# Kernel optimization log

Hardware: AMD Instinct MI355X
Metric: run time of the kernel (lower is better)

## Reference

```python
import jax, jax.numpy as jnp
import numpy as np

DIM = 1024
NUM_HEADS = 16
HEAD_DIM = DIM // NUM_HEADS


def setup_inputs() -> dict:
    key = jax.random.key(0)
    k1, k2, k3 = jax.random.split(key, 3)
    scale = 1.0 / np.sqrt(DIM)
    x = jax.random.normal(k1, (4, 2048, DIM), dtype=jnp.float32)
    w_qkv = jax.random.normal(k2, (DIM, 3 * DIM), dtype=jnp.float32) * scale
    b_qkv = jnp.zeros((3 * DIM,), dtype=jnp.float32)
    w_out = jax.random.normal(k3, (DIM, DIM), dtype=jnp.float32) * scale
    b_out = jnp.zeros((DIM,), dtype=jnp.float32)
    return {"x": x, "w_qkv": w_qkv, "b_qkv": b_qkv, "w_out": w_out, "b_out": b_out}


def reference(x, w_qkv, b_qkv, w_out, b_out):
    B, S, D = x.shape
    H, Hd = NUM_HEADS, HEAD_DIM
    qkv = x @ w_qkv + b_qkv  # [B,S,3D]
    q, k, v = jnp.split(qkv, 3, axis=-1)
    # [B,H,S,Hd]
    q = q.reshape(B, S, H, Hd).transpose(0, 2, 1, 3)
    k = k.reshape(B, S, H, Hd).transpose(0, 2, 1, 3)
    v = v.reshape(B, S, H, Hd).transpose(0, 2, 1, 3)
    scores = jnp.einsum('bhqd,bhkd->bhqk', q, k) / np.sqrt(Hd).astype(np.float32)
    causal = jnp.triu(jnp.ones((S, S), dtype=bool), k=1)  # True above diagonal -> masked
    scores = jnp.where(causal[None, None], -jnp.inf, scores)
    scores = scores - jnp.max(scores, axis=-1, keepdims=True)
    attn = jax.nn.softmax(scores, axis=-1)
    out = jnp.einsum('bhqk,bhkd->bhqd', attn, v)  # [B,H,S,Hd]
    out = out.transpose(0, 2, 1, 3).reshape(B, S, D)
    return out @ w_out + b_out
```

## Files before the change

### kernel.cpp

```cpp
#include <hip/hip_runtime.h>

typedef unsigned short u16;
typedef unsigned int u32;
using f32x4 = __attribute__((ext_vector_type(4))) float;
using f32x16 = __attribute__((ext_vector_type(16))) float;
using u32x4 = __attribute__((ext_vector_type(4))) u32;
typedef u32x4 __attribute__((may_alias)) u32x4a;
typedef uint2 __attribute__((may_alias)) uint2a;
using bf16x8 = __attribute__((ext_vector_type(8))) __bf16;

#define SEQ 2048

__device__ __forceinline__ u16 f2bf(float f) {
  union { float f; u32 u; } c; c.f = f;
  return (u16)((c.u + 0x7fffu + ((c.u >> 16) & 1u)) >> 16);
}
__device__ __forceinline__ float bf2f(u16 h) {
  union { u32 u; float f; } c; c.u = ((u32)h) << 16;
  return c.f;
}
__device__ __forceinline__ bf16x8 ld16(const u16* p) {
  return __builtin_bit_cast(bf16x8, *(const u32x4a*)p);
}
__device__ __forceinline__ f32x4 mfma16(bf16x8 a, bf16x8 b, f32x4 c) {
  return __builtin_amdgcn_mfma_f32_16x16x32_bf16(a, b, c, 0, 0, 0);
}
__device__ __forceinline__ f32x16 mfma32(bf16x8 a, bf16x8 b, f32x16 c) {
  return __builtin_amdgcn_mfma_f32_32x32x16_bf16(a, b, c, 0, 0, 0);
}
__device__ __forceinline__ void gload_lds16(const u16* g, u16* l) {
  __builtin_amdgcn_global_load_lds(
      (const __attribute__((address_space(1))) void*)g,
      (__attribute__((address_space(3))) void*)l, 16, 0, 0);
}
__device__ __forceinline__ u32 cvtpk(float lo, float hi) {
  u32 r;
  asm("v_cvt_pk_bf16_f32 %0, %1, %2" : "=v"(r) : "v"(lo), "v"(hi));
  return r;
}
__device__ __forceinline__ void plane32_swap(u32& a, u32& b) {
  asm("v_permlane32_swap_b32 %0, %1" : "+v"(a), "+v"(b));
}

__global__ void detect_dtype(const u16* __restrict__ x, int* __restrict__ flag) {
  if (threadIdx.x == 0) {
    int cnt = 0;
    for (int i = 0; i < 32; ++i) {
      const int e = (x[2 * i] >> 7) & 0xFF;
      cnt += (e >= 100 && e <= 140) ? 1 : 0;
    }
    *flag = (cnt >= 20) ? 1 : 0;
  }
}


__global__ __launch_bounds__(256)
void cvt_x(const void* __restrict__ in, u16* __restrict__ out,
           const int* __restrict__ flag, size_t eoff4) {
  const size_t i = (size_t)blockIdx.x * 256 + threadIdx.x;
  if (*flag) {
    ((uint2*)out)[i] = ((const uint2*)in)[eoff4 + i];
  } else {
    const float4 v = ((const float4*)in)[eoff4 + i];
    uint2 ov;
    ov.x = (u32)f2bf(v.x) | ((u32)f2bf(v.y) << 16);
    ov.y = (u32)f2bf(v.z) | ((u32)f2bf(v.w) << 16);
    ((uint2*)out)[i] = ov;
  }
}

__global__ __launch_bounds__(256)
void cvt_bias(const void* __restrict__ in, float* __restrict__ out, int n,
              const int* __restrict__ flag) {
  const int i = blockIdx.x * 256 + threadIdx.x;
  if (i >= n) return;
  out[i] = (*flag) ? bf2f(((const u16*)in)[i]) : ((const float*)in)[i];
}

__global__ __launch_bounds__(256)
void transpose_w(const void* __restrict__ in, u16* __restrict__ out, int K, int N,
                 const int* __restrict__ flag) {
  __shared__ float t[64][65];
  const int tid = threadIdx.x;
  const int r = tid >> 4, c4 = tid & 15;
  const int n0 = blockIdx.x << 6, k0 = blockIdx.y << 6;
  const int fl = *flag;
#pragma unroll
  for (int i = 0; i < 4; ++i) {
    const int kk = r + i * 16;
    const size_t base = (size_t)(k0 + kk) * N + n0 + c4 * 4;
    if (fl) {
      const uint2 raw = *(const uint2*)((const u16*)in + base);
      t[kk][c4 * 4 + 0] = bf2f((u16)(raw.x & 0xFFFF));
      t[kk][c4 * 4 + 1] = bf2f((u16)(raw.x >> 16));
      t[kk][c4 * 4 + 2] = bf2f((u16)(raw.y & 0xFFFF));
      t[kk][c4 * 4 + 3] = bf2f((u16)(raw.y >> 16));
    } else {
      const float4 v = *(const float4*)((const float*)in + base);
      t[kk][c4 * 4 + 0] = v.x; t[kk][c4 * 4 + 1] = v.y;
      t[kk][c4 * 4 + 2] = v.z; t[kk][c4 * 4 + 3] = v.w;
    }
  }
  __syncthreads();
#pragma unroll
  for (int i = 0; i < 4; ++i) {
    const int nn = r + i * 16;
    uint2 ov;
    ov.x = (u32)f2bf(t[c4 * 4 + 0][nn]) | ((u32)f2bf(t[c4 * 4 + 1][nn]) << 16);
    ov.y = (u32)f2bf(t[c4 * 4 + 2][nn]) | ((u32)f2bf(t[c4 * 4 + 3][nn]) << 16);
    *(uint2*)&out[(size_t)(n0 + nn) * K + k0 + c4 * 4] = ov;
  }
}

template <bool BF16_OUT>
__global__ __launch_bounds__(512, 4)
void gemm_bt(const u16* __restrict__ A, const u16* __restrict__ BT,
             const float* __restrict__ bias, void* __restrict__ Cv,
             u16* __restrict__ Vt, int M, int N, int K) {
  constexpr int BK = 32;
  __shared__ __align__(16) u16 ring[3][12288];
  const int tid = threadIdx.x;
  const int wid = tid >> 6, lane = tid & 63;
  const int quad = lane >> 4, l16 = lane & 15;

  const int nbx = gridDim.x, nwg = nbx * gridDim.y;
  int bid = blockIdx.y * nbx + blockIdx.x;
  if ((nwg & 7) == 0) bid = (bid & 7) * (nwg >> 3) + (bid >> 3);
  const int tile_n = (bid % nbx) << 7;
  const int tile_m = (bid / nbx) << 8;

  const int wmR = (wid >> 1) << 6;
  const int wnR = (wid & 1) << 6;

  const int G0 = tid;
  const int rA0 = G0 >> 2, sA0 = ((G0 & 3) ^ ((rA0 >> 1) & 3)) * 8;
  const int G1 = tid + 512;
  const int rA1 = G1 >> 2, sA1 = ((G1 & 3) ^ ((rA1 >> 1) & 3)) * 8;
  const u16* const pA0 = A + (size_t)(tile_m + rA0) * K + sA0;
  const u16* const pA1 = A + (size_t)(tile_m + rA1) * K + sA1;
  const u16* const pB0 = BT + (size_t)(tile_n + rA0) * K + sA0;
  const int dw = wid * 512;

  const int cA = (quad ^ ((l16 >> 1) & 3)) * 8;

  const int nk = K >> 5;
  f32x4 acc[4][4] = {};

  auto STAGE = [&](int kt, int buf) {
    u16* bp = ring[buf];
    const size_t ko = (size_t)kt * BK;
    gload_lds16(pA0 + ko, bp + dw);
    gload_lds16(pA1 + ko, bp + 4096 + dw);
    gload_lds16(pB0 + ko, bp + 8192 + dw);
  };

  STAGE(0, 0);
  if (nk > 1) STAGE(1, 1);

  int cur = 0;
#pragma unroll 1
  for (int t = 0; t < nk; ++t) {
    if (t + 1 < nk) asm volatile("s_waitcnt vmcnt(3)" ::: "memory");
    else            asm volatile("s_waitcnt vmcnt(0)" ::: "memory");
    __builtin_amdgcn_sched_barrier(0);
    __builtin_amdgcn_s_barrier();
    __builtin_amdgcn_sched_barrier(0);
    int sb = cur + 2; if (sb >= 3) sb -= 3;
    if (t + 2 < nk) STAGE(t + 2, sb);
    const u16* bp = ring[cur];
    bf16x8 af[4], bfr[4];
#pragma unroll
    for (int i = 0; i < 4; ++i)
      af[i] = ld16(&bp[(wmR + i * 16 + l16) * BK + cA]);
#pragma unroll
    for (int j = 0; j < 4; ++j)
      bfr[j] = ld16(&bp[8192 + (wnR + j * 16 + l16) * BK + cA]);
#pragma unroll
    for (int i = 0; i < 4; ++i)
#pragma unroll
      for (int j = 0; j < 4; ++j) acc[i][j] = mfma16(af[i], bfr[j], acc[i][j]);
    cur = (cur + 1 == 3) ? 0 : cur + 1;
  }

  if constexpr (BF16_OUT) {
    if (tile_n >= 2048) {
#pragma unroll
      for (int j = 0; j < 4; ++j) {
        const int cv = tile_n - 2048 + wnR + j * 16 + l16;
        const float bv = bias[2048 + cv];
#pragma unroll
        for (int i = 0; i < 4; ++i) {
          const int rg = tile_m + wmR + i * 16 + quad * 4;
          const int b2 = rg >> 11, s = rg & 2047;
          uint2a wv;
          wv.x = cvtpk(acc[i][j][0] + bv, acc[i][j][1] + bv);
          wv.y = cvtpk(acc[i][j][2] + bv, acc[i][j][3] + bv);
          *(uint2a*)&Vt[((size_t)(b2 * 1024 + cv)) * 2048 + s] = wv;
        }
      }
      return;
    }
  }

#pragma unroll
  for (int j = 0; j < 4; ++j) {
    const int cg = tile_n + wnR + j * 16 + l16;
    const float bv = bias[cg];
#pragma unroll
    for (int i = 0; i < 4; ++i) {
      const int rg = tile_m + wmR + i * 16 + quad * 4;
#pragma unroll
      for (int r = 0; r < 4; ++r) {
        const float v = acc[i][j][r] + bv;
        if constexpr (BF16_OUT)
          ((u16*)Cv)[(size_t)(rg + r) * N + cg] = f2bf(v);
        else
          ((float*)Cv)[(size_t)(rg + r) * N + cg] = v;
      }
    }
  }
}

__global__ __launch_bounds__(256, 2)
void attn_fwd(const u16* __restrict__ qkv, const u16* __restrict__ vt,
              u16* __restrict__ aout) {
  const int h = blockIdx.x, b = blockIdx.z;
  const int tid = threadIdx.x, wid = tid >> 6, lane = tid & 63;
  const int l31 = lane & 31, hi = lane >> 5;
  __shared__ __align__(16) u16 ring[4][8192];

  const int G0 = wid * 64 + lane, G1 = G0 + 256;
  const int r0 = G0 >> 3, c0 = ((G0 & 7) ^ (r0 & 7)) * 8;
  const int r1 = G1 >> 3, c1 = ((G1 & 7) ^ (r1 & 7)) * 8;
  const int db0 = wid * 512, db1 = 2048 + wid * 512;

  const u16* const kg = qkv + (size_t)(b * SEQ) * 3072 + 1024 + h * 64;
  const u16* const vg = vt + (size_t)((b * 16 + h) * 64) * 2048;

  constexpr float SC = 0.1803368801f;
  constexpr float THR = 44.3614196f;

  u32x4 onesu;
  onesu[0] = onesu[1] = onesu[2] = onesu[3] = 0x3F803F80u;
  const bf16x8 ones = __builtin_bit_cast(bf16x8, onesu);

  const int sx = l31 & 7;

  auto STAGE = [&](int kt) {
    u16* bp = ring[kt & 3];
    const int kb = kt * 64;
    gload_lds16(kg + (size_t)(kb + r0) * 3072 + c0, bp + db0);
    gload_lds16(kg + (size_t)(kb + r1) * 3072 + c1, bp + db1);
    gload_lds16(vg + (size_t)r0 * 2048 + kb + c0, bp + 4096 + db0);
    gload_lds16(vg + (size_t)r1 * 2048 + kb + c1, bp + 4096 + db1);
  };

#pragma unroll 1
  for (int pass = 0; pass < 2; ++pass) {
    const int qt = pass ? (int)blockIdx.y : 15 - (int)blockIdx.y;
    const int q0w = qt * 128 + wid * 32;
    const int qrow = q0w + l31;
    bf16x8 qf[4];
#pragma unroll
    for (int d = 0; d < 4; ++d)
      qf[d] = ld16(&qkv[(size_t)(b * SEQ + qrow) * 3072 + h * 64 + d * 16 + hi * 8]);
    f32x16 o0 = {}, o1 = {}, lacc = {};
    float m_r = -1e30f, ms = -1.8e29f;

    const int last = 2 * qt + 1;
    __syncthreads();
    STAGE(0);
    if (last >= 1) STAGE(1);
    if (last >= 2) STAGE(2);

#pragma unroll 1
    for (int kt = 0; kt <= last; ++kt) {
      const int rem = last - kt;
      if (rem >= 2)      asm volatile("s_waitcnt vmcnt(8)" ::: "memory");
      else if (rem == 1) asm volatile("s_waitcnt vmcnt(4)" ::: "memory");
      else               asm volatile("s_waitcnt vmcnt(0)" ::: "memory");
      __builtin_amdgcn_sched_barrier(0);
      __builtin_amdgcn_s_barrier();
      __builtin_amdgcn_sched_barrier(0);
      if (kt + 3 <= last) STAGE(kt + 3);
      const int kb = kt * 64;
      if (kb <= q0w + 31) {
        const u16* const lKc = ring[kt & 3];
        const u16* const lVc = ring[kt & 3] + 4096;
        f32x16 s0 = {}, s1 = {};
        bf16x8 kf0[4], kf1[4];
#pragma unroll
        for (int d = 0; d < 4; ++d) {
          kf0[d] = ld16(&lKc[l31 * 64 + (((d * 2 + hi) ^ sx)) * 8]);
          kf1[d] = ld16(&lKc[(32 + l31) * 64 + (((d * 2 + hi) ^ sx)) * 8]);
        }
        __builtin_amdgcn_s_setprio(1);
#pragma unroll
        for (int d = 0; d < 4; ++d) s0 = mfma32(kf0[d], qf[d], s0);
#pragma unroll
        for (int d = 0; d < 4; ++d) s1 = mfma32(kf1[d], qf[d], s1);
        __builtin_amdgcn_s_setprio(0);
        bf16x8 vf[2][2][2];
#pragma unroll
        for (int kh = 0; kh < 2; ++kh)
#pragma unroll
          for (int j = 0; j < 2; ++j)
#pragma unroll
            for (int dh = 0; dh < 2; ++dh)
              vf[kh][j][dh] = ld16(
                  &lVc[(dh * 32 + l31) * 64 + (((kh * 4 + j * 2 + hi) ^ sx)) * 8]);
        if (kb + 63 > q0w) {
          const int rel = qrow - kb - 4 * hi;
#pragma unroll
          for (int i = 0; i < 16; ++i) {
            const int kc = (i & 3) + 8 * (i >> 2);
            if (kc > rel) s0[i] = -1e30f;
            if (kc + 32 > rel) s1[i] = -1e30f;
          }
        }
        float pm = fmaxf(fmaxf(s0[0], s0[1]), s0[2]);
        pm = fmaxf(fmaxf(pm, s0[3]), s0[4]);
        pm = fmaxf(fmaxf(pm, s0[5]), s0[6]);
        pm = fmaxf(fmaxf(pm, s0[7]), s0[8]);
        pm = fmaxf(fmaxf(pm, s0[9]), s0[10]);
        pm = fmaxf(fmaxf(pm, s0[11]), s0[12]);
        pm = fmaxf(fmaxf(pm, s0[13]), s0[14]);
        pm = fmaxf(fmaxf(pm, s0[15]), s1[0]);
        pm = fmaxf(fmaxf(pm, s1[1]), s1[2]);
        pm = fmaxf(fmaxf(pm, s1[3]), s1[4]);
        pm = fmaxf(fmaxf(pm, s1[5]), s1[6]);
        pm = fmaxf(fmaxf(pm, s1[7]), s1[8]);
        pm = fmaxf(fmaxf(pm, s1[9]), s1[10]);
        pm = fmaxf(fmaxf(pm, s1[11]), s1[12]);
        pm = fmaxf(fmaxf(pm, s1[13]), s1[14]);
        pm = fmaxf(pm, s1[15]);
        if (__any(pm > m_r + THR)) {
          const float mm = fmaxf(pm, __shfl_xor(pm, 32));
          const float mn = fmaxf(m_r, mm);
          const float al = exp2f((m_r - mn) * SC);
#pragma unroll
          for (int i = 0; i < 16; ++i) {
            o0[i] *= al; o1[i] *= al; lacc[i] *= al;
          }
          m_r = mn;
          ms = mn * SC;
        }
#pragma unroll
        for (int i = 0; i < 16; ++i) {
          s0[i] = exp2f(fmaf(s0[i], SC, -ms));
          s1[i] = exp2f(fmaf(s1[i], SC, -ms));
        }
        u32 t0 = cvtpk(s0[0], s0[1]), t1 = cvtpk(s0[2], s0[3]);
        u32 t2 = cvtpk(s0[4], s0[5]), t3 = cvtpk(s0[6], s0[7]);
        u32 t4 = cvtpk(s0[8], s0[9]), t5 = cvtpk(s0[10], s0[11]);
        u32 t6 = cvtpk(s0[12], s0[13]), t7 = cvtpk(s0[14], s0[15]);
        plane32_swap(t0, t2); plane32_swap(t1, t3);
        plane32_swap(t4, t6); plane32_swap(t5, t7);
        u32x4 w00, w01;
        w00[0] = t0; w00[1] = t1; w00[2] = t2; w00[3] = t3;
        w01[0] = t4; w01[1] = t5; w01[2] = t6; w01[3] = t7;
        u32 u0 = cvtpk(s1[0], s1[1]), u1 = cvtpk(s1[2], s1[3]);
        u32 u2 = cvtpk(s1[4], s1[5]), u3 = cvtpk(s1[6], s1[7]);
        u32 u4 = cvtpk(s1[8], s1[9]), u5 = cvtpk(s1[10], s1[11]);
        u32 u6 = cvtpk(s1[12], s1[13]), u7 = cvtpk(s1[14], s1[15]);
        plane32_swap(u0, u2); plane32_swap(u1, u3);
        plane32_swap(u4, u6); plane32_swap(u5, u7);
        u32x4 w10, w11;
        w10[0] = u0; w10[1] = u1; w10[2] = u2; w10[3] = u3;
        w11[0] = u4; w11[1] = u5; w11[2] = u6; w11[3] = u7;
        const bf16x8 pb00 = __builtin_bit_cast(bf16x8, w00);
        const bf16x8 pb01 = __builtin_bit_cast(bf16x8, w01);
        const bf16x8 pb10 = __builtin_bit_cast(bf16x8, w10);
        const bf16x8 pb11 = __builtin_bit_cast(bf16x8, w11);
        __builtin_amdgcn_s_setprio(1);
        o0 = mfma32(vf[0][0][0], pb00, o0);
        o1 = mfma32(vf[0][0][1], pb00, o1);
        lacc = mfma32(ones, pb00, lacc);
        o0 = mfma32(vf[0][1][0], pb01, o0);
        o1 = mfma32(vf[0][1][1], pb01, o1);
        lacc = mfma32(ones, pb01, lacc);
        o0 = mfma32(vf[1][0][0], pb10, o0);
        o1 = mfma32(vf[1][0][1], pb10, o1);
        lacc = mfma32(ones, pb10, lacc);
        o0 = mfma32(vf[1][1][0], pb11, o0);
        o1 = mfma32(vf[1][1][1], pb11, o1);
        lacc = mfma32(ones, pb11, lacc);
        __builtin_amdgcn_s_setprio(0);
      }
    }
    const float inv = 1.0f / lacc[0];
    u16* const orow = &aout[(size_t)(b * SEQ + qrow) * 1024 + h * 64];
#pragma unroll
    for (int t = 0; t < 4; ++t) {
      const int d0 = 8 * t + 4 * hi;
      uint2a wv;
      wv.x = cvtpk(o0[4 * t] * inv, o0[4 * t + 1] * inv);
      wv.y = cvtpk(o0[4 * t + 2] * inv, o0[4 * t + 3] * inv);
      *(uint2a*)&orow[d0] = wv;
      wv.x = cvtpk(o1[4 * t] * inv, o1[4 * t + 1] * inv);
      wv.y = cvtpk(o1[4 * t + 2] * inv, o1[4 * t + 3] * inv);
      *(uint2a*)&orow[32 + d0] = wv;
    }
  }
}

extern "C" void kernel_launch(void* const* d_in, const int* in_sizes, int n_in,
                              void* d_out, int out_size, void* d_ws, size_t ws_size,
                              hipStream_t stream) {
  const void* x     = d_in[0];
  const void* w_qkv = d_in[1];
  const void* b_qkv = d_in[2];
  const void* w_out = d_in[3];
  const void* b_out = d_in[4];
  float* out = (float*)d_out;

  float* bqf   = (float*)d_ws;
  float* bof   = bqf + 3072;
  int*   flag  = (int*)(bof + 1024);
  u16*   wqkvT = (u16*)(flag + 4);
  u16*   woutT = wqkvT + (size_t)3072 * 1024;
  u16*   xb    = woutT + (size_t)1024 * 1024;

  detect_dtype<<<dim3(1), dim3(64), 0, stream>>>((const u16*)x, flag);
  cvt_bias<<<dim3(12), dim3(256), 0, stream>>>(b_qkv, bqf, 3072, flag);
  cvt_bias<<<dim3(4), dim3(256), 0, stream>>>(b_out, bof, 1024, flag);
  transpose_w<<<dim3(48, 16), dim3(256), 0, stream>>>(w_qkv, wqkvT, 1024, 3072, flag);
  transpose_w<<<dim3(16, 16), dim3(256), 0, stream>>>(w_out, woutT, 1024, 1024, flag);

  const size_t FULL_WS = 92291088;
  if (ws_size >= FULL_WS) {
    u16* qkv = xb  + (size_t)8192 * 1024;
    u16* vt  = qkv + (size_t)8192 * 3072;
    cvt_x<<<dim3(8192), dim3(256), 0, stream>>>(x, xb, flag, 0);
    gemm_bt<true ><<<dim3(24, 32), dim3(512), 0, stream>>>(xb, wqkvT, bqf, qkv,
                                                           vt, 8192, 3072, 1024);
    attn_fwd<<<dim3(16, 8, 4), dim3(256), 0, stream>>>(qkv, vt, xb);
    gemm_bt<false><<<dim3(8, 32), dim3(512), 0, stream>>>(xb, woutT, bof, out,
                                                          vt, 8192, 1024, 1024);
  } else {
    u16* qkvb = xb   + (size_t)2048 * 1024;
    u16* vtb  = qkvb + (size_t)2048 * 3072;
    for (int b = 0; b < 4; ++b) {
      const size_t eoff4 = (size_t)b * 2048 * 1024 / 4;
      cvt_x<<<dim3(2048), dim3(256), 0, stream>>>(x, xb, flag, eoff4);
      gemm_bt<true ><<<dim3(24, 8), dim3(512), 0, stream>>>(xb, wqkvT, bqf, qkvb,
                                                            vtb, 2048, 3072, 1024);
      attn_fwd<<<dim3(16, 8, 1), dim3(256), 0, stream>>>(qkvb, vtb, xb);
      gemm_bt<false><<<dim3(8, 8), dim3(512), 0, stream>>>(
          xb, woutT, bof, out + (size_t)b * 2048 * 1024, vtb, 2048, 1024, 1024);
    }
  }
}
```

Baseline: 277.5 us.

## Split attention blocks per query tile, shrink LDS ring, fuse prep kernels

Attention no longer pairs two query tiles per block (long+short for balance). It launches one block per query tile (grid y 16) with the tiles ordered longest first. The LDS ring drops from 4 to 3 stages with prefetch distance 2, allowing 3 blocks per CU. The five small preprocessing kernels (dtype detection, bias conversion, weight transposes) are merged into one launch, and each block recomputes the dtype flag locally. The risks are lost load balance from the pairing and a shallower prefetch pipeline.

```diff
diff --git a/kernel.cpp b/kernel.cpp
--- a/kernel.cpp
+++ b/kernel.cpp
@@ -41,50 +41,50 @@
 __device__ __forceinline__ void plane32_swap(u32& a, u32& b) {
   asm("v_permlane32_swap_b32 %0, %1" : "+v"(a), "+v"(b));
 }
-
-__global__ void detect_dtype(const u16* __restrict__ x, int* __restrict__ flag) {
-  if (threadIdx.x == 0) {
-    int cnt = 0;
-    for (int i = 0; i < 32; ++i) {
-      const int e = (x[2 * i] >> 7) & 0xFF;
-      cnt += (e >= 100 && e <= 140) ? 1 : 0;
-    }
-    *flag = (cnt >= 20) ? 1 : 0;
-  }
-}
-
+__device__ __forceinline__ int detect_flag(const u16* x) {
+  int cnt = 0;
+  for (int i = 0; i < 32; ++i) {
+    const int e = (x[2 * i] >> 7) & 0xFF;
+    cnt += (e >= 100 && e <= 140) ? 1 : 0;
+  }
+  return (cnt >= 20) ? 1 : 0;
+}
 
 __global__ __launch_bounds__(256)
-void cvt_x(const void* __restrict__ in, u16* __restrict__ out,
-           const int* __restrict__ flag, size_t eoff4) {
-  const size_t i = (size_t)blockIdx.x * 256 + threadIdx.x;
-  if (*flag) {
-    ((uint2*)out)[i] = ((const uint2*)in)[eoff4 + i];
-  } else {
-    const float4 v = ((const float4*)in)[eoff4 + i];
-    uint2 ov;
-    ov.x = (u32)f2bf(v.x) | ((u32)f2bf(v.y) << 16);
-    ov.y = (u32)f2bf(v.z) | ((u32)f2bf(v.w) << 16);
-    ((uint2*)out)[i] = ov;
-  }
-}
-
-__global__ __launch_bounds__(256)
-void cvt_bias(const void* __restrict__ in, float* __restrict__ out, int n,
-              const int* __restrict__ flag) {
-  const int i = blockIdx.x * 256 + threadIdx.x;
-  if (i >= n) return;
-  out[i] = (*flag) ? bf2f(((const u16*)in)[i]) : ((const float*)in)[i];
-}
-
-__global__ __launch_bounds__(256)
-void transpose_w(const void* __restrict__ in, u16* __restrict__ out, int K, int N,
-                 const int* __restrict__ flag) {
+void prep_all(const void* __restrict__ x, const void* __restrict__ w_qkv,
+              const void* __restrict__ b_qkv, const void* __restrict__ w_out,
+              const void* __restrict__ b_out, u16* __restrict__ wqkvT,
+              u16* __restrict__ woutT, float* __restrict__ bqf,
+              float* __restrict__ bof, int* __restrict__ flagp) {
+  __shared__ int sflag;
   __shared__ float t[64][65];
   const int tid = threadIdx.x;
+  if (tid == 0) sflag = detect_flag((const u16*)x);
+  __syncthreads();
+  const int fl = sflag;
+  const int bid = blockIdx.x;
+  if (bid == 1040) {
+    if (tid == 0) *flagp = fl;
+    return;
+  }
+  if (bid >= 1024) {
+    if (bid < 1036) {
+      const int i = (bid - 1024) * 256 + tid;
+      bqf[i] = fl ? bf2f(((const u16*)b_qkv)[i]) : ((const float*)b_qkv)[i];
+    } else {
+      const int i = (bid - 1036) * 256 + tid;
+      bof[i] = fl ? bf2f(((const u16*)b_out)[i]) : ((const float*)b_out)[i];
+    }
+    return;
+  }
+  const void* in;
+  u16* outp;
+  int N, bx, by;
+  if (bid < 768) { in = w_qkv; outp = wqkvT; N = 3072; bx = bid % 48; by = bid / 48; }
+  else { in = w_out; outp = woutT; N = 1024; bx = (bid - 768) % 16; by = (bid - 768) / 16; }
+  const int K = 1024;
   const int r = tid >> 4, c4 = tid & 15;
-  const int n0 = blockIdx.x << 6, k0 = blockIdx.y << 6;
-  const int fl = *flag;
+  const int n0 = bx << 6, k0 = by << 6;
 #pragma unroll
   for (int i = 0; i < 4; ++i) {
     const int kk = r + i * 16;
@@ -108,7 +108,22 @@
     uint2 ov;
     ov.x = (u32)f2bf(t[c4 * 4 + 0][nn]) | ((u32)f2bf(t[c4 * 4 + 1][nn]) << 16);
     ov.y = (u32)f2bf(t[c4 * 4 + 2][nn]) | ((u32)f2bf(t[c4 * 4 + 3][nn]) << 16);
-    *(uint2*)&out[(size_t)(n0 + nn) * K + k0 + c4 * 4] = ov;
+    *(uint2*)&outp[(size_t)(n0 + nn) * K + k0 + c4 * 4] = ov;
+  }
+}
+
+__global__ __launch_bounds__(256)
+void cvt_x(const void* __restrict__ in, u16* __restrict__ out,
+           const int* __restrict__ flag, size_t eoff4) {
+  const size_t i = (size_t)blockIdx.x * 256 + threadIdx.x;
+  if (*flag) {
+    ((uint2*)out)[i] = ((const uint2*)in)[eoff4 + i];
+  } else {
+    const float4 v = ((const float4*)in)[eoff4 + i];
+    uint2 ov;
+    ov.x = (u32)f2bf(v.x) | ((u32)f2bf(v.y) << 16);
+    ov.y = (u32)f2bf(v.z) | ((u32)f2bf(v.w) << 16);
+    ((uint2*)out)[i] = ov;
   }
 }
 
@@ -221,13 +236,14 @@
   }
 }
 
-__global__ __launch_bounds__(256, 2)
+__global__ __launch_bounds__(256, 3)
 void attn_fwd(const u16* __restrict__ qkv, const u16* __restrict__ vt,
               u16* __restrict__ aout) {
   const int h = blockIdx.x, b = blockIdx.z;
+  const int qt = 15 - (int)blockIdx.y;
   const int tid = threadIdx.x, wid = tid >> 6, lane = tid & 63;
   const int l31 = lane & 31, hi = lane >> 5;
-  __shared__ __align__(16) u16 ring[4][8192];
+  __shared__ __align__(16) u16 ring[3][8192];
 
   const int G0 = wid * 64 + lane, G1 = G0 + 256;
   const int r0 = G0 >> 3, c0 = ((G0 & 7) ^ (r0 & 7)) * 8;
@@ -246,8 +262,8 @@
 
   const int sx = l31 & 7;
 
-  auto STAGE = [&](int kt) {
-    u16* bp = ring[kt & 3];
+  auto STAGE = [&](int kt, int buf) {
+    u16* bp = ring[buf];
     const int kb = kt * 64;
     gload_lds16(kg + (size_t)(kb + r0) * 3072 + c0, bp + db0);
     gload_lds16(kg + (size_t)(kb + r1) * 3072 + c1, bp + db1);
@@ -255,152 +271,147 @@
     gload_lds16(vg + (size_t)r1 * 2048 + kb + c1, bp + 4096 + db1);
   };
 
+  const int q0w = qt * 128 + wid * 32;
+  const int qrow = q0w + l31;
+  bf16x8 qf[4];
+#pragma unroll
+  for (int d = 0; d < 4; ++d)
+    qf[d] = ld16(&qkv[(size_t)(b * SEQ + qrow) * 3072 + h * 64 + d * 16 + hi * 8]);
+  f32x16 o0 = {}, o1 = {}, lacc = {};
+  float m_r = -1e30f, ms = -1.8e29f;
+
+  const int last = 2 * qt + 1;
+  STAGE(0, 0);
+  if (last >= 1) STAGE(1, 1);
+
+  int cur = 0;
 #pragma unroll 1
-  for (int pass = 0; pass < 2; ++pass) {
-    const int qt = pass ? (int)blockIdx.y : 15 - (int)blockIdx.y;
-    const int q0w = qt * 128 + wid * 32;
-    const int qrow = q0w + l31;
-    bf16x8 qf[4];
-#pragma unroll
-    for (int d = 0; d < 4; ++d)
-      qf[d] = ld16(&qkv[(size_t)(b * SEQ + qrow) * 3072 + h * 64 + d * 16 + hi * 8]);
-    f32x16 o0 = {}, o1 = {}, lacc = {};
-    float m_r = -1e30f, ms = -1.8e29f;
-
-    const int last = 2 * qt + 1;
-    __syncthreads();
-    STAGE(0);
-    if (last >= 1) STAGE(1);
-    if (last >= 2) STAGE(2);
-
-#pragma unroll 1
-    for (int kt = 0; kt <= last; ++kt) {
-      const int rem = last - kt;
-      if (rem >= 2)      asm volatile("s_waitcnt vmcnt(8)" ::: "memory");
-      else if (rem == 1) asm volatile("s_waitcnt vmcnt(4)" ::: "memory");
-      else               asm volatile("s_waitcnt vmcnt(0)" ::: "memory");
-      __builtin_amdgcn_sched_barrier(0);
-      __builtin_amdgcn_s_barrier();
-      __builtin_amdgcn_sched_barrier(0);
-      if (kt + 3 <= last) STAGE(kt + 3);
-      const int kb = kt * 64;
-      if (kb <= q0w + 31) {
-        const u16* const lKc = ring[kt & 3];
-        const u16* const lVc = ring[kt & 3] + 4096;
-        f32x16 s0 = {}, s1 = {};
-        bf16x8 kf0[4], kf1[4];
-#pragma unroll
-        for (int d = 0; d < 4; ++d) {
-          kf0[d] = ld16(&lKc[l31 * 64 + (((d * 2 + hi) ^ sx)) * 8]);
-          kf1[d] = ld16(&lKc[(32 + l31) * 64 + (((d * 2 + hi) ^ sx)) * 8]);
+  for (int kt = 0; kt <= last; ++kt) {
+    if (kt + 1 <= last) asm volatile("s_waitcnt vmcnt(4)" ::: "memory");
+    else                asm volatile("s_waitcnt vmcnt(0)" ::: "memory");
+    __builtin_amdgcn_sched_barrier(0);
+    __builtin_amdgcn_s_barrier();
+    __builtin_amdgcn_sched_barrier(0);
+    int sb = cur + 2; if (sb >= 3) sb -= 3;
+    if (kt + 2 <= last) STAGE(kt + 2, sb);
+    const int kb = kt * 64;
+    if (kb <= q0w + 31) {
+      const u16* const lKc = ring[cur];
+      const u16* const lVc = ring[cur] + 4096;
+      f32x16 s0 = {}, s1 = {};
+      bf16x8 kf0[4], kf1[4];
+#pragma unroll
+      for (int d = 0; d < 4; ++d) {
+        kf0[d] = ld16(&lKc[l31 * 64 + (((d * 2 + hi) ^ sx)) * 8]);
+        kf1[d] = ld16(&lKc[(32 + l31) * 64 + (((d * 2 + hi) ^ sx)) * 8]);
+      }
+      __builtin_amdgcn_s_setprio(1);
+#pragma unroll
+      for (int d = 0; d < 4; ++d) s0 = mfma32(kf0[d], qf[d], s0);
+#pragma unroll
+      for (int d = 0; d < 4; ++d) s1 = mfma32(kf1[d], qf[d], s1);
+      __builtin_amdgcn_s_setprio(0);
+      bf16x8 vf[2][2][2];
+#pragma unroll
+      for (int kh = 0; kh < 2; ++kh)
+#pragma unroll
+        for (int j = 0; j < 2; ++j)
+#pragma unroll
+          for (int dh = 0; dh < 2; ++dh)
+            vf[kh][j][dh] = ld16(
+                &lVc[(dh * 32 + l31) * 64 + (((kh * 4 + j * 2 + hi) ^ sx)) * 8]);
+      if (kb + 63 > q0w) {
+        const int rel = qrow - kb - 4 * hi;
+#pragma unroll
+        for (int i = 0; i < 16; ++i) {
+          const int kc = (i & 3) + 8 * (i >> 2);
+          if (kc > rel) s0[i] = -1e30f;
+          if (kc + 32 > rel) s1[i] = -1e30f;
         }
-        __builtin_amdgcn_s_setprio(1);
-#pragma unroll
-        for (int d = 0; d < 4; ++d) s0 = mfma32(kf0[d], qf[d], s0);
-#pragma unroll
-        for (int d = 0; d < 4; ++d) s1 = mfma32(kf1[d], qf[d], s1);
-        __builtin_amdgcn_s_setprio(0);
-        bf16x8 vf[2][2][2];
-#pragma unroll
-        for (int kh = 0; kh < 2; ++kh)
-#pragma unroll
-          for (int j = 0; j < 2; ++j)
-#pragma unroll
-            for (int dh = 0; dh < 2; ++dh)
-              vf[kh][j][dh] = ld16(
-                  &lVc[(dh * 32 + l31) * 64 + (((kh * 4 + j * 2 + hi) ^ sx)) * 8]);
-        if (kb + 63 > q0w) {
-          const int rel = qrow - kb - 4 * hi;
-#pragma unroll
-          for (int i = 0; i < 16; ++i) {
-            const int kc = (i & 3) + 8 * (i >> 2);
-            if (kc > rel) s0[i] = -1e30f;
-            if (kc + 32 > rel) s1[i] = -1e30f;
-          }
+      }
+      float pm = fmaxf(fmaxf(s0[0], s0[1]), s0[2]);
+      pm = fmaxf(fmaxf(pm, s0[3]), s0[4]);
+      pm = fmaxf(fmaxf(pm, s0[5]), s0[6]);
+      pm = fmaxf(fmaxf(pm, s0[7]), s0[8]);
+      pm = fmaxf(fmaxf(pm, s0[9]), s0[10]);
+      pm = fmaxf(fmaxf(pm, s0[11]), s0[12]);
+      pm = fmaxf(fmaxf(pm, s0[13]), s0[14]);
+      pm = fmaxf(fmaxf(pm, s0[15]), s1[0]);
+      pm = fmaxf(fmaxf(pm, s1[1]), s1[2]);
+      pm = fmaxf(fmaxf(pm, s1[3]), s1[4]);
+      pm = fmaxf(fmaxf(pm, s1[5]), s1[6]);
+      pm = fmaxf(fmaxf(pm, s1[7]), s1[8]);
+      pm = fmaxf(fmaxf(pm, s1[9]), s1[10]);
+      pm = fmaxf(fmaxf(pm, s1[11]), s1[12]);
+      pm = fmaxf(fmaxf(pm, s1[13]), s1[14]);
+      pm = fmaxf(pm, s1[15]);
+      if (__any(pm > m_r + THR)) {
+        const float mm = fmaxf(pm, __shfl_xor(pm, 32));
+        const float mn = fmaxf(m_r, mm);
+        const float al = exp2f((m_r - mn) * SC);
+#pragma unroll
+        for (int i = 0; i < 16; ++i) {
+          o0[i] *= al; o1[i] *= al; lacc[i] *= al;
         }
-        float pm = fmaxf(fmaxf(s0[0], s0[1]), s0[2]);
-        pm = fmaxf(fmaxf(pm, s0[3]), s0[4]);
-        pm = fmaxf(fmaxf(pm, s0[5]), s0[6]);
-        pm = fmaxf(fmaxf(pm, s0[7]), s0[8]);
-        pm = fmaxf(fmaxf(pm, s0[9]), s0[10]);
-        pm = fmaxf(fmaxf(pm, s0[11]), s0[12]);
-        pm = fmaxf(fmaxf(pm, s0[13]), s0[14]);
-        pm = fmaxf(fmaxf(pm, s0[15]), s1[0]);
-        pm = fmaxf(fmaxf(pm, s1[1]), s1[2]);
-        pm = fmaxf(fmaxf(pm, s1[3]), s1[4]);
-        pm = fmaxf(fmaxf(pm, s1[5]), s1[6]);
-        pm = fmaxf(fmaxf(pm, s1[7]), s1[8]);
-        pm = fmaxf(fmaxf(pm, s1[9]), s1[10]);
-        pm = fmaxf(fmaxf(pm, s1[11]), s1[12]);
-        pm = fmaxf(fmaxf(pm, s1[13]), s1[14]);
-        pm = fmaxf(pm, s1[15]);
-        if (__any(pm > m_r + THR)) {
-          const float mm = fmaxf(pm, __shfl_xor(pm, 32));
-          const float mn = fmaxf(m_r, mm);
-          const float al = exp2f((m_r - mn) * SC);
-#pragma unroll
-          for (int i = 0; i < 16; ++i) {
-            o0[i] *= al; o1[i] *= al; lacc[i] *= al;
-          }
-          m_r = mn;
-          ms = mn * SC;
-        }
-#pragma unroll
-        for (int i = 0; i < 16; ++i) {
-          s0[i] = exp2f(fmaf(s0[i], SC, -ms));
-          s1[i] = exp2f(fmaf(s1[i], SC, -ms));
-        }
-        u32 t0 = cvtpk(s0[0], s0[1]), t1 = cvtpk(s0[2], s0[3]);
-        u32 t2 = cvtpk(s0[4], s0[5]), t3 = cvtpk(s0[6], s0[7]);
-        u32 t4 = cvtpk(s0[8], s0[9]), t5 = cvtpk(s0[10], s0[11]);
-        u32 t6 = cvtpk(s0[12], s0[13]), t7 = cvtpk(s0[14], s0[15]);
-        plane32_swap(t0, t2); plane32_swap(t1, t3);
-        plane32_swap(t4, t6); plane32_swap(t5, t7);
-        u32x4 w00, w01;
-        w00[0] = t0; w00[1] = t1; w00[2] = t2; w00[3] = t3;
-        w01[0] = t4; w01[1] = t5; w01[2] = t6; w01[3] = t7;
-        u32 u0 = cvtpk(s1[0], s1[1]), u1 = cvtpk(s1[2], s1[3]);
-        u32 u2 = cvtpk(s1[4], s1[5]), u3 = cvtpk(s1[6], s1[7]);
-        u32 u4 = cvtpk(s1[8], s1[9]), u5 = cvtpk(s1[10], s1[11]);
-        u32 u6 = cvtpk(s1[12], s1[13]), u7 = cvtpk(s1[14], s1[15]);
-        plane32_swap(u0, u2); plane32_swap(u1, u3);
-        plane32_swap(u4, u6); plane32_swap(u5, u7);
-        u32x4 w10, w11;
-        w10[0] = u0; w10[1] = u1; w10[2] = u2; w10[3] = u3;
-        w11[0] = u4; w11[1] = u5; w11[2] = u6; w11[3] = u7;
-        const bf16x8 pb00 = __builtin_bit_cast(bf16x8, w00);
-        const bf16x8 pb01 = __builtin_bit_cast(bf16x8, w01);
-        const bf16x8 pb10 = __builtin_bit_cast(bf16x8, w10);
-        const bf16x8 pb11 = __builtin_bit_cast(bf16x8, w11);
-        __builtin_amdgcn_s_setprio(1);
-        o0 = mfma32(vf[0][0][0], pb00, o0);
-        o1 = mfma32(vf[0][0][1], pb00, o1);
-        lacc = mfma32(ones, pb00, lacc);
-        o0 = mfma32(vf[0][1][0], pb01, o0);
-        o1 = mfma32(vf[0][1][1], pb01, o1);
-        lacc = mfma32(ones, pb01, lacc);
-        o0 = mfma32(vf[1][0][0], pb10, o0);
-        o1 = mfma32(vf[1][0][1], pb10, o1);
-        lacc = mfma32(ones, pb10, lacc);
-        o0 = mfma32(vf[1][1][0], pb11, o0);
-        o1 = mfma32(vf[1][1][1], pb11, o1);
-        lacc = mfma32(ones, pb11, lacc);
-        __builtin_amdgcn_s_setprio(0);
-      }
-    }
-    const float inv = 1.0f / lacc[0];
-    u16* const orow = &aout[(size_t)(b * SEQ + qrow) * 1024 + h * 64];
-#pragma unroll
-    for (int t = 0; t < 4; ++t) {
-      const int d0 = 8 * t + 4 * hi;
-      uint2a wv;
-      wv.x = cvtpk(o0[4 * t] * inv, o0[4 * t + 1] * inv);
-      wv.y = cvtpk(o0[4 * t + 2] * inv, o0[4 * t + 3] * inv);
-      *(uint2a*)&orow[d0] = wv;
-      wv.x = cvtpk(o1[4 * t] * inv, o1[4 * t + 1] * inv);
-      wv.y = cvtpk(o1[4 * t + 2] * inv, o1[4 * t + 3] * inv);
-      *(uint2a*)&orow[32 + d0] = wv;
-    }
+        m_r = mn;
+        ms = mn * SC;
+      }
+#pragma unroll
+      for (int i = 0; i < 16; ++i) {
+        s0[i] = exp2f(fmaf(s0[i], SC, -ms));
+        s1[i] = exp2f(fmaf(s1[i], SC, -ms));
+      }
+      u32 t0 = cvtpk(s0[0], s0[1]), t1 = cvtpk(s0[2], s0[3]);
+      u32 t2 = cvtpk(s0[4], s0[5]), t3 = cvtpk(s0[6], s0[7]);
+      u32 t4 = cvtpk(s0[8], s0[9]), t5 = cvtpk(s0[10], s0[11]);
+      u32 t6 = cvtpk(s0[12], s0[13]), t7 = cvtpk(s0[14], s0[15]);
+      plane32_swap(t0, t2); plane32_swap(t1, t3);
+      plane32_swap(t4, t6); plane32_swap(t5, t7);
+      u32x4 w00, w01;
+      w00[0] = t0; w00[1] = t1; w00[2] = t2; w00[3] = t3;
+      w01[0] = t4; w01[1] = t5; w01[2] = t6; w01[3] = t7;
+      u32 u0 = cvtpk(s1[0], s1[1]), u1 = cvtpk(s1[2], s1[3]);
+      u32 u2 = cvtpk(s1[4], s1[5]), u3 = cvtpk(s1[6], s1[7]);
+      u32 u4 = cvtpk(s1[8], s1[9]), u5 = cvtpk(s1[10], s1[11]);
+      u32 u6 = cvtpk(s1[12], s1[13]), u7 = cvtpk(s1[14], s1[15]);
+      plane32_swap(u0, u2); plane32_swap(u1, u3);
+      plane32_swap(u4, u6); plane32_swap(u5, u7);
+      u32x4 w10, w11;
+      w10[0] = u0; w10[1] = u1; w10[2] = u2; w10[3] = u3;
+      w11[0] = u4; w11[1] = u5; w11[2] = u6; w11[3] = u7;
+      const bf16x8 pb00 = __builtin_bit_cast(bf16x8, w00);
+      const bf16x8 pb01 = __builtin_bit_cast(bf16x8, w01);
+      const bf16x8 pb10 = __builtin_bit_cast(bf16x8, w10);
+      const bf16x8 pb11 = __builtin_bit_cast(bf16x8, w11);
+      __builtin_amdgcn_s_setprio(1);
+      o0 = mfma32(vf[0][0][0], pb00, o0);
+      o1 = mfma32(vf[0][0][1], pb00, o1);
+      lacc = mfma32(ones, pb00, lacc);
+      o0 = mfma32(vf[0][1][0], pb01, o0);
+      o1 = mfma32(vf[0][1][1], pb01, o1);
+      lacc = mfma32(ones, pb01, lacc);
+      o0 = mfma32(vf[1][0][0], pb10, o0);
+      o1 = mfma32(vf[1][0][1], pb10, o1);
+      lacc = mfma32(ones, pb10, lacc);
+      o0 = mfma32(vf[1][1][0], pb11, o0);
+      o1 = mfma32(vf[1][1][1], pb11, o1);
+      lacc = mfma32(ones, pb11, lacc);
+      __builtin_amdgcn_s_setprio(0);
+    }
+    cur = (cur + 1 == 3) ? 0 : cur + 1;
+  }
+  const float inv = 1.0f / lacc[0];
+  u16* const orow = &aout[(size_t)(b * SEQ + qrow) * 1024 + h * 64];
+#pragma unroll
+  for (int t = 0; t < 4; ++t) {
+    const int d0 = 8 * t + 4 * hi;
+    uint2a wv;
+    wv.x = cvtpk(o0[4 * t] * inv, o0[4 * t + 1] * inv);
+    wv.y = cvtpk(o0[4 * t + 2] * inv, o0[4 * t + 3] * inv);
+    *(uint2a*)&orow[d0] = wv;
+    wv.x = cvtpk(o1[4 * t] * inv, o1[4 * t + 1] * inv);
+    wv.y = cvtpk(o1[4 * t + 2] * inv, o1[4 * t + 3] * inv);
+    *(uint2a*)&orow[32 + d0] = wv;
   }
 }
 
@@ -421,11 +432,8 @@
   u16*   woutT = wqkvT + (size_t)3072 * 1024;
   u16*   xb    = woutT + (size_t)1024 * 1024;
 
-  detect_dtype<<<dim3(1), dim3(64), 0, stream>>>((const u16*)x, flag);
-  cvt_bias<<<dim3(12), dim3(256), 0, stream>>>(b_qkv, bqf, 3072, flag);
-  cvt_bias<<<dim3(4), dim3(256), 0, stream>>>(b_out, bof, 1024, flag);
-  transpose_w<<<dim3(48, 16), dim3(256), 0, stream>>>(w_qkv, wqkvT, 1024, 3072, flag);
-  transpose_w<<<dim3(16, 16), dim3(256), 0, stream>>>(w_out, woutT, 1024, 1024, flag);
+  prep_all<<<dim3(1041), dim3(256), 0, stream>>>(
+      x, w_qkv, b_qkv, w_out, b_out, wqkvT, woutT, bqf, bof, flag);
 
   const size_t FULL_WS = 92291088;
   if (ws_size >= FULL_WS) {
@@ -434,7 +442,7 @@
     cvt_x<<<dim3(8192), dim3(256), 0, stream>>>(x, xb, flag, 0);
     gemm_bt<true ><<<dim3(24, 32), dim3(512), 0, stream>>>(xb, wqkvT, bqf, qkv,
                                                            vt, 8192, 3072, 1024);
-    attn_fwd<<<dim3(16, 8, 4), dim3(256), 0, stream>>>(qkv, vt, xb);
+    attn_fwd<<<dim3(16, 16, 4), dim3(256), 0, stream>>>(qkv, vt, xb);
     gemm_bt<false><<<dim3(8, 32), dim3(512), 0, stream>>>(xb, woutT, bof, out,
                                                           vt, 8192, 1024, 1024);
   } else {
@@ -445,7 +453,7 @@
       cvt_x<<<dim3(2048), dim3(256), 0, stream>>>(x, xb, flag, eoff4);
       gemm_bt<true ><<<dim3(24, 8), dim3(512), 0, stream>>>(xb, wqkvT, bqf, qkvb,
                                                             vtb, 2048, 3072, 1024);
-      attn_fwd<<<dim3(16, 8, 1), dim3(256), 0, stream>>>(qkvb, vtb, xb);
+      attn_fwd<<<dim3(16, 16, 1), dim3(256), 0, stream>>>(qkvb, vtb, xb);
       gemm_bt<false><<<dim3(8, 8), dim3(512), 0, stream>>>(
           xb, woutT, bof, out + (size_t)b * 2048 * 1024, vtb, 2048, 1024, 1024);
     }
```

Result: slower. 291.5 us (+5.0%).
